# Kernel tuning notes

Measured on AMD Instinct MI355X. Metric: run time of the kernel, lower is better.

The kernel has to match this reference:

```python
import jax, jax.numpy as jnp
import numpy as np
from jax import lax

B, IN_C, Q_C, V_C, H, W = 16, 3, 8, 16, 224, 224
K = 7  # static conv kernel size


def _conv(x, w, stride=2, pad=3):
    # x: [N, Cin, H, W], w: [Cout, Cin, kh, kw]
    return lax.conv_general_dilated(
        x, w, (stride, stride), [(pad, pad), (pad, pad)],
        dimension_numbers=("NCHW", "OIHW", "NCHW"))


def _dyn_conv(inp, w):
    # per-sample dynamic conv: inp [C, H, W], w [O, C, kh, kw] -> [O, oh, ow]
    return _conv(inp[None], w, stride=2, pad=3)[0]


def setup_inputs() -> dict:
    key = jax.random.key(0)
    ks = jax.random.split(key, 8)
    x = jax.random.normal(ks[0], (B, IN_C, H, W), dtype=jnp.float32)
    # q_conv_params: input_channel x (weight [q, in, 7, 7], bias [q])
    Wq = jax.random.normal(ks[1], (IN_C, Q_C, IN_C, K, K), dtype=jnp.float32)
    bq = jax.random.normal(ks[2], (IN_C, Q_C), dtype=jnp.float32)
    # k_conv_paramss: input_channel x v_channel x (weight [q, in, 7, 7], bias [q])
    Wk = jax.random.normal(ks[3], (IN_C, V_C, Q_C, IN_C, K, K), dtype=jnp.float32)
    bk = jax.random.normal(ks[4], (IN_C, V_C, Q_C), dtype=jnp.float32)
    # v_conv_param: (weight [v, in, 7, 7], bias [v])
    Wv = jax.random.normal(ks[5], (V_C, IN_C, K, K), dtype=jnp.float32)
    bv = jax.random.normal(ks[6], (V_C,), dtype=jnp.float32)
    return {"x": x, "Wq": Wq, "bq": bq, "Wk": Wk, "bk": bk, "Wv": Wv, "bv": bv}


def reference(x, Wq, bq, Wk, bk, Wv, bv):
    b = x.shape[0]
    in_c, q_c = Wq.shape[0], Wq.shape[1]
    v_c = Wk.shape[1]
    # q: stack of input_channel static convs -> one grouped-by-output conv
    q = _conv(x, Wq.reshape(in_c * q_c, *Wq.shape[2:])) \
        + bq.reshape(-1)[None, :, None, None]
    h2, w2 = q.shape[-2], q.shape[-1]  # 112, 112
    q = q.reshape(b, in_c, q_c, h2, w2)
    # ks: input_channel x v_channel static convs fused into one conv
    kmap = _conv(x, Wk.reshape(in_c * v_c * q_c, *Wk.shape[3:])) \
        + bk.reshape(-1)[None, :, None, None]
    kmap = kmap.reshape(b, in_c, v_c, q_c, h2, w2)
    # a: per (batch, in_c) dynamic conv with feature maps as 112x112 kernels
    # input q[b,i] [q_c, h2, w2], weight kmap[b,i] [v_c, q_c, h2, w2] -> [v_c, 4, 4]
    a = jax.vmap(jax.vmap(_dyn_conv))(q, kmap)  # [B, in_c, v_c, 4, 4]
    # v: static conv
    v = _conv(x, Wv) + bv[None, :, None, None]  # [B, v_c, h2, w2]
    # o: per-batch dynamic conv with a[b] as kernel -> [B, in_c, 58, 58]
    o = jax.vmap(_dyn_conv)(v, a)
    return o
```

## Files before the change

### kernel.cpp

```cpp
#include <hip/hip_runtime.h>
#include <hip/hip_bf16.h>

#define BATCH 16
#define IN_C 3
#define Q_C 8
#define V_C 16
#define HH 224
#define WW 224
#define KK 7

#define XPH 230
#define XPW 232
#define QPH 118
#define QPW 120
#define QP_PLANE (QPH*QPW)
#define QP_QSTRIDE (Q_C*QP_PLANE)

#define PT_MB    202
#define PT2_CHUNKS (BATCH*IN_C*PT_MB*112)
#define PT2_N    ((size_t)PT2_CHUNKS*8)

#define PLANES_N (BATCH*7*IN_C*XPH*QPW)
#define VPAD_N   (BATCH*V_C*QPH*QPW)
#define QPADS_N  (BATCH*IN_C*QP_QSTRIDE)
#define D_N      (BATCH*160*384)
#define SPLITS   16
#define DPART_N  (SPLITS*D_N)
#define OUT_N    (BATCH*IN_C*58*58)
#define AW_N     (4*48*192)

#define ZQ_CHUNKS (BATCH*IN_C*Q_C*6*15)
#define ZV_CHUNKS (BATCH*V_C*6*30)

typedef __attribute__((ext_vector_type(8))) short bf16x8;
typedef __attribute__((ext_vector_type(4))) float f32x4;
typedef __attribute__((ext_vector_type(4))) unsigned short u16x4;

struct __attribute__((packed, aligned(4))) uint4_a4 { uint4 v; };
struct __attribute__((packed, aligned(4))) float4_a4 { float4 v; };

static __device__ inline unsigned short f2b(float f) {
    __hip_bfloat16 h = __float2bfloat16(f);
    return *reinterpret_cast<unsigned short*>(&h);
}
static __device__ inline float b2f(unsigned short u) {
    unsigned int v = ((unsigned int)u) << 16;
    return __builtin_bit_cast(float, v);
}
static __device__ inline bf16x8 ld16(const unsigned short* p) {
    return __builtin_bit_cast(bf16x8, *(const uint4*)p);
}

__global__ __launch_bounds__(256) void kXT(const float* __restrict__ x,
                                           unsigned short* __restrict__ planes,
                                           unsigned short* __restrict__ pT2) {
    int blk = blockIdx.x;
    int r0 = blk % 29;
    int t0 = blk / 29;
    int ci = t0 % IN_C;
    int b  = t0 / IN_C;
    int tid = threadIdx.x;

    __shared__ unsigned short xl[8][240];

    const float* xb = x + (size_t)(b * IN_C + ci) * (HH * WW);
    for (int idx = tid; idx < 8 * 240; idx += 256) {
        int row8 = idx / 240, c = idx % 240;
        int r = 8 * r0 + row8 - 3;
        int cc = c - 3;
        float val = 0.0f;
        if (r >= 0 && r < HH && cc >= 0 && cc < WW)
            val = xb[(size_t)r * WW + cc];
        xl[row8][c] = f2b(val);
    }
    __syncthreads();

    for (int t2 = tid; t2 < 840; t2 += 256) {
        int ko = t2 % 15;
        int t3 = t2 / 15;
        int row8 = t3 % 8;
        int dx = t3 / 8;
        int prow = 8 * r0 + row8;
        if (prow >= XPH) continue;
        unsigned short pk[8];
        if (ko < 14) {
            #pragma unroll
            for (int j = 0; j < 8; ++j)
                pk[j] = xl[row8][16 * ko + 2 * j + dx];
        } else {
            #pragma unroll
            for (int j = 0; j < 8; ++j) pk[j] = 0;
        }
        unsigned short* dst = planes
            + ((size_t)((b * 7 + dx) * IN_C + ci) * XPH + prow) * QPW + 8 * ko;
        *(uint4*)dst = *(const uint4*)pk;
    }

    for (int t2 = tid; t2 < 784; t2 += 256) {
        int kc  = t2 % 112;
        int mbr = t2 / 112;
        int mb = 7 * r0 + mbr;
        if (mb >= PT_MB) continue;
        unsigned short pk[8];
        #pragma unroll
        for (int j = 0; j < 8; ++j) {
            int mrel = 8 * mbr + j;
            int row8 = mrel / 7;
            int dxm  = mrel - 7 * row8;
            pk[j] = xl[row8][2 * kc + dxm];
        }
        unsigned short* dst = pT2 + ((size_t)((b * IN_C + ci) * PT_MB + mb) * 112 + kc) * 8;
        *(uint4*)dst = *(const uint4*)pk;
    }
}

__global__ __launch_bounds__(256) void kW(const float* __restrict__ Wq,
                                          const float* __restrict__ Wv,
                                          unsigned short* __restrict__ Aw2) {
    int idx = blockIdx.x * 256 + threadIdx.x;
    if (idx >= AW_N) return;
    int n = idx % 192;
    int t3 = idx / 192;
    int ch = t3 % 48;
    int p4 = t3 / 48;
    int ci = n / 64;
    int t  = (n % 64) - 2 * p4;
    float v = 0.0f;
    if (ch < 40 && t >= 0 && t < 49) {
        int k = ci * 49 + t;
        v = (ch < 24) ? Wq[(size_t)ch * 147 + k] : Wv[(size_t)(ch - 24) * 147 + k];
    }
    Aw2[idx] = f2b(v);
}

__global__ __launch_bounds__(256) void kZ(unsigned short* __restrict__ qpadS,
                                          float* __restrict__ vpad) {
    int idx = blockIdx.x * 256 + threadIdx.x;
    if (idx >= ZQ_CHUNKS + ZV_CHUNKS) return;
    uint4 z = uint4{0, 0, 0, 0};
    if (idx < ZQ_CHUNKS) {
        int ko = idx % 15;
        int t2 = idx / 15;
        int r6 = t2 % 6;
        int plane = t2 / 6;
        int row = (r6 < 3) ? r6 : (112 + r6);
        *(uint4*)(qpadS + (size_t)plane * QP_PLANE + (size_t)row * QPW + 8 * ko) = z;
    } else {
        int j = idx - ZQ_CHUNKS;
        int ko = j % 30;
        int t2 = j / 30;
        int r6 = t2 % 6;
        int plane = t2 / 6;
        int row = (r6 < 3) ? r6 : (112 + r6);
        *(uint4*)((char*)(vpad + (size_t)plane * QP_PLANE + (size_t)row * QPW) + 16 * ko) = z;
    }
}

__global__ __launch_bounds__(256) void kA(const unsigned short* __restrict__ pT2,
                                          const unsigned short* __restrict__ Aw2,
                                          const float* __restrict__ bq,
                                          const float* __restrict__ bv,
                                          unsigned short* __restrict__ qpadS,
                                          float* __restrict__ vpad) {
    int g = blockIdx.x;
    int r8 = g & 7, q8 = g >> 3;
    int b  = r8 + 8 * (q8 / 28);
    int yq = q8 % 28;
    int w  = threadIdx.x >> 6;
    int yo = yq * 4 + w;
    int lane = threadIdx.x & 63;
    int cl = lane & 15, kq = lane >> 4;

    __shared__ unsigned short qs[4][24][120];
    __shared__ float          vs[4][16][120];

    int m14 = 14 * yo;
    int p4  = (m14 >> 1) & 3;
    int ms8 = m14 >> 3;

    const unsigned short* AwP = Aw2 + (size_t)p4 * (48 * 192);
    bf16x8 af[3][6];
    #pragma unroll
    for (int mt = 0; mt < 3; ++mt)
        #pragma unroll
        for (int s = 0; s < 6; ++s)
            af[mt][s] = ld16(AwP + (size_t)(mt * 16 + cl) * 192 + s * 32 + kq * 8);

    f32x4 acc[3][7];
    #pragma unroll
    for (int mt = 0; mt < 3; ++mt)
        #pragma unroll
        for (int nt = 0; nt < 7; ++nt)
            acc[mt][nt] = f32x4{0.f, 0.f, 0.f, 0.f};

    #pragma unroll
    for (int s = 0; s < 6; ++s) {
        int ci = s >> 1;
        int mb = ms8 + kq + 4 * (s & 1);
        const unsigned short* bp = pT2
            + ((size_t)((b * IN_C + ci) * PT_MB + mb) * 112) * 8;
        bf16x8 bfr[7];
        #pragma unroll
        for (int nt = 0; nt < 7; ++nt)
            bfr[nt] = ld16(bp + (size_t)(nt * 16 + cl) * 8);
        #pragma unroll
        for (int nt = 0; nt < 7; ++nt)
            #pragma unroll
            for (int mt = 0; mt < 3; ++mt)
                acc[mt][nt] = __builtin_amdgcn_mfma_f32_16x16x32_bf16(af[mt][s], bfr[nt], acc[mt][nt], 0, 0, 0);
    }

    float bias[3][4];
    #pragma unroll
    for (int mt = 0; mt < 3; ++mt)
        #pragma unroll
        for (int r = 0; r < 4; ++r) {
            int ch = mt * 16 + kq * 4 + r;
            bias[mt][r] = (ch < 24) ? bq[ch] : (ch < 40 ? bv[ch - 24] : 0.0f);
        }

    for (int i = lane; i < 24 * 8; i += 64) {
        int ch = i / 8, c = i % 8;
        qs[w][ch][(c < 3) ? c : (112 + c)] = 0;
    }
    for (int i = lane; i < 16 * 8; i += 64) {
        int ch = i / 8, c = i % 8;
        vs[w][ch][(c < 3) ? c : (112 + c)] = 0.0f;
    }

    #pragma unroll
    for (int mt = 0; mt < 3; ++mt) {
        #pragma unroll
        for (int nt = 0; nt < 7; ++nt) {
            int kc = nt * 16 + cl;
            #pragma unroll
            for (int r = 0; r < 4; ++r) {
                int ch = mt * 16 + kq * 4 + r;
                float val = acc[mt][nt][r] + bias[mt][r];
                if (ch < 24) qs[w][ch][3 + kc] = f2b(val);
                else if (ch < 40) vs[w][ch - 24][3 + kc] = val;
            }
        }
    }
    __syncthreads();

    int orow = yo + 3;
    for (int i = lane; i < 24 * 15; i += 64) {
        int ch = i / 15, ko = i % 15;
        int icq = ch >> 3, qc = ch & 7;
        *(uint4*)(qpadS + (size_t)((b * 3 + icq) * 8 + qc) * QP_PLANE
                  + (size_t)orow * QPW + 8 * ko) = *(const uint4*)(&qs[w][ch][8 * ko]);
    }
    for (int i = lane; i < 16 * 30; i += 64) {
        int ch = i / 30, ko = i % 30;
        *(float4*)((char*)(vpad + (size_t)(b * 16 + ch) * QP_PLANE
                           + (size_t)orow * QPW) + 16 * ko) =
            *(const float4*)((const char*)(&vs[w][ch][0]) + 16 * ko);
    }
}

__global__ __launch_bounds__(512, 4) void kC(const unsigned short* __restrict__ planes,
                                             const unsigned short* __restrict__ qpadS,
                                             unsigned short* __restrict__ Dpart) {
    int blk = blockIdx.x;
    int b   = blk & 15;
    int nh  = (blk >> 4) & 1;
    int yc  = blk >> 5;
    int tid = threadIdx.x;
    int w = tid >> 6, lane = tid & 63;
    int tt = lane & 15, kq = lane >> 4;
    int th = tt >> 2, tw = tt & 3;

    __shared__ union {
        uint4 bs[80 * 17];
        unsigned short dq[80 * 392];
    } sm;

    int nreal = nh ? 67 : 80;

    if (tid < nreal * 3) {
        int nl = tid / 3, j2 = tid % 3;
        sm.bs[nl * 17 + 14 + j2] = uint4{0, 0, 0, 0};
    } else if (nh == 1) {
        int t2 = tid - nreal * 3;
        if (t2 < 13 * 17) {
            int nl = 67 + t2 / 17, ss = t2 % 17;
            uint4 v = (ss < 14) ? uint4{0x3F803F80u, 0x3F803F80u, 0x3F803F80u, 0x3F803F80u}
                                : uint4{0, 0, 0, 0};
            sm.bs[nl * 17 + ss] = v;
        }
    }

    int nch = nreal * 14;
    int soff[3];
    int sdst[3];
    bool sact[3];
    #pragma unroll
    for (int i = 0; i < 3; ++i) {
        int c = tid + 512 * i;
        sact[i] = (c < nch);
        int cc2 = sact[i] ? c : 0;
        int nl = cc2 / 14;
        int k0 = (cc2 % 14) * 8;
        int n = nh * 80 + nl;
        int ci = n / 49;
        int rr = n % 49;
        int dy = rr / 7;
        int dx = rr % 7;
        soff[i] = (((b * 7 + dx) * IN_C + ci) * XPH + dy) * QPW + k0;
        sdst[i] = nl * 17 + (k0 >> 3);
    }

    const unsigned short* abase[3];
    #pragma unroll
    for (int j = 0; j < 3; ++j) {
        int tile = w * 3 + j;
        int ic = tile >> 3, qc = tile & 7;
        abase[j] = qpadS + (size_t)(b * IN_C + ic) * QP_QSTRIDE + qc * QP_PLANE
                 + (2 * th) * QPW + 2 * tw;
    }

    f32x4 acc[3][5];
    #pragma unroll
    for (int j = 0; j < 3; ++j)
        #pragma unroll
        for (int nt = 0; nt < 5; ++nt)
            acc[j][nt] = f32x4{0.f, 0.f, 0.f, 0.f};

    uint4 pf[3];
    int yo0 = yc * 7;
    #pragma unroll
    for (int i = 0; i < 3; ++i)
        if (sact[i]) pf[i] = *(const uint4*)(planes + soff[i] + yo0 * 240);

    for (int ry = 0; ry < 7; ++ry) {
        int yo = yc * 7 + ry;
        __syncthreads();
        #pragma unroll
        for (int i = 0; i < 3; ++i)
            if (sact[i]) sm.bs[sdst[i]] = pf[i];
        __syncthreads();
        if (ry < 6) {
            #pragma unroll
            for (int i = 0; i < 3; ++i)
                if (sact[i]) pf[i] = *(const uint4*)(planes + soff[i] + (yo + 1) * 240);
        }
        #pragma unroll
        for (int s = 0; s < 4; ++s) {
            int k = 32 * s + kq * 8;
            int xs = (k < 112) ? k : 96;
            bf16x8 af[3];
            #pragma unroll
            for (int j = 0; j < 3; ++j)
                af[j] = __builtin_bit_cast(bf16x8,
                    ((const uint4_a4*)(abase[j] + yo * QPW + xs))->v);
            #pragma unroll
            for (int nt = 0; nt < 5; ++nt) {
                bf16x8 bf = __builtin_bit_cast(bf16x8, sm.bs[(nt * 16 + tt) * 17 + 4 * s + kq]);
                #pragma unroll
                for (int j = 0; j < 3; ++j)
                    acc[j][nt] = __builtin_amdgcn_mfma_f32_16x16x32_bf16(af[j], bf, acc[j][nt], 0, 0, 0);
            }
        }
    }

    __syncthreads();
    #pragma unroll
    for (int j = 0; j < 3; ++j) {
        int tile = w * 3 + j;
        int mb = tile * 16 + kq * 4;
        #pragma unroll
        for (int nt = 0; nt < 5; ++nt) {
            int nl = nt * 16 + tt;
            u16x4 pk;
            pk.x = f2b(acc[j][nt][0]);
            pk.y = f2b(acc[j][nt][1]);
            pk.z = f2b(acc[j][nt][2]);
            pk.w = f2b(acc[j][nt][3]);
            *(u16x4*)(&sm.dq[nl * 392 + mb]) = pk;
        }
    }
    __syncthreads();
    unsigned short* Dp = Dpart + (size_t)(yc * 16 + b) * (160 * 384);
    for (int c = tid; c < 80 * 48; c += 512) {
        int nl = c / 48, ms = c % 48;
        *(uint4*)(Dp + (size_t)(nh * 80 + nl) * 384 + ms * 8) =
            *(const uint4*)(&sm.dq[nl * 392 + ms * 8]);
    }
}

__global__ __launch_bounds__(256) void kR(const unsigned short* __restrict__ Dpart,
                                          float* __restrict__ Df) {
    int idx = blockIdx.x * 256 + threadIdx.x;
    float4 s = float4{0.f, 0.f, 0.f, 0.f};
    #pragma unroll
    for (int yc = 0; yc < SPLITS; ++yc) {
        u16x4 v = *(const u16x4*)(Dpart + (size_t)yc * D_N + 4 * (size_t)idx);
        s.x += b2f(v.x);
        s.y += b2f(v.y);
        s.z += b2f(v.z);
        s.w += b2f(v.w);
    }
    *(float4*)(Df + 4 * (size_t)idx) = s;
}

__global__ __launch_bounds__(256) void kE(const float* __restrict__ Df,
                                          const float* __restrict__ Wk,
                                          const float* __restrict__ bk,
                                          float* __restrict__ a_out) {
    int blk = blockIdx.x;
    int bi = blk >> 4;
    int v  = blk & 15;
    int ic = bi % IN_C;
    int b  = bi / IN_C;
    int tid = threadIdx.x;
    int t  = tid & 15;
    int rl = tid >> 4;
    const float* Dbase = Df + (size_t)b * (160 * 384);
    const float* WkI = Wk + (size_t)(ic * V_C + v) * (Q_C * 147);
    const float* bkI = bk + (ic * V_C + v) * Q_C;
    float s = 0.0f;
    for (int qc = 0; qc < Q_C; ++qc) {
        const float* wrow = WkI + qc * 147;
        int mcol = ic * 128 + qc * 16 + t;
        #pragma unroll
        for (int j = 0; j < 10; ++j) {
            int r = rl + 16 * j;
            if (r < 148) {
                float wv = (r < 147) ? wrow[r] : bkI[qc];
                s = fmaf(wv, Dbase[(size_t)r * 384 + mcol], s);
            }
        }
    }
    __shared__ float red[256];
    red[tid] = s;
    __syncthreads();
    if (tid < 16) {
        float acc2 = 0.f;
        #pragma unroll
        for (int k2 = 0; k2 < 16; ++k2) acc2 += red[k2 * 16 + tid];
        a_out[(size_t)blk * 16 + tid] = acc2;
    }
}

__global__ __launch_bounds__(256) void kO(const float* __restrict__ vpad,
                                          const float* __restrict__ a,
                                          float* __restrict__ out) {
    int idx = blockIdx.x * 256 + threadIdx.x;
    if (idx >= OUT_N) return;
    int ow = idx % 58;
    int t = idx / 58;
    int oh = t % 58; t /= 58;
    int ic = t % IN_C;
    int b  = t / IN_C;
    const float* ab = a + (size_t)(b * IN_C + ic) * (V_C * 16);
    float s = 0.0f;
    for (int vc = 0; vc < V_C; ++vc) {
        const float* vrow = vpad + ((size_t)(b * V_C + vc) * QPH + 2 * oh) * QPW + 2 * ow;
        const float* ar = ab + vc * 16;
        #pragma unroll
        for (int kh = 0; kh < 4; ++kh) {
            float4 xv = ((const float4_a4*)(vrow + kh * QPW))->v;
            s = fmaf(xv.x, ar[kh * 4 + 0], s);
            s = fmaf(xv.y, ar[kh * 4 + 1], s);
            s = fmaf(xv.z, ar[kh * 4 + 2], s);
            s = fmaf(xv.w, ar[kh * 4 + 3], s);
        }
    }
    out[idx] = s;
}

extern "C" void kernel_launch(void* const* d_in, const int* in_sizes, int n_in,
                              void* d_out, int out_size, void* d_ws, size_t ws_size,
                              hipStream_t stream) {
    (void)in_sizes; (void)n_in; (void)out_size; (void)ws_size;
    const float* x  = (const float*)d_in[0];
    const float* Wq = (const float*)d_in[1];
    const float* bq = (const float*)d_in[2];
    const float* Wk = (const float*)d_in[3];
    const float* bk = (const float*)d_in[4];
    const float* Wv = (const float*)d_in[5];
    const float* bv = (const float*)d_in[6];
    float* out = (float*)d_out;

    char* p = (char*)d_ws;
    unsigned short* pT2   = (unsigned short*)p;
    unsigned short* Dpart = (unsigned short*)p;
    p += (size_t)DPART_N * 2;
    unsigned short* planes = (unsigned short*)p;        p += (size_t)PLANES_N * 2;
    float*          vpad   = (float*)p;                 p += (size_t)VPAD_N * 4;
    unsigned short* qpadS  = (unsigned short*)p;        p += (size_t)QPADS_N * 2;
    float*          Df     = (float*)p;                 p += (size_t)D_N * 4;
    unsigned short* Aw2    = (unsigned short*)p;        p += (size_t)AW_N * 2;
    float*          a      = (float*)p;

    kXT<<<BATCH * IN_C * 29, 256, 0, stream>>>(x, planes, pT2);
    kW<<<(AW_N + 255) / 256, 256, 0, stream>>>(Wq, Wv, Aw2);
    kZ<<<(ZQ_CHUNKS + ZV_CHUNKS + 255) / 256, 256, 0, stream>>>(qpadS, vpad);
    kA<<<448, 256, 0, stream>>>(pT2, Aw2, bq, bv, qpadS, vpad);
    kC<<<SPLITS * 2 * 16, 512, 0, stream>>>(planes, qpadS, Dpart);
    kR<<<D_N / 4 / 256, 256, 0, stream>>>(Dpart, Df);
    kE<<<BATCH * IN_C * V_C, 256, 0, stream>>>(Df, Wk, bk, a);
    kO<<<(OUT_N + 255) / 256, 256, 0, stream>>>(vpad, a, out);
}
```

Baseline: 175.5 us.

## Double-buffer B rows in kC and merge weight-pack and zero-pad kernels

kC now stages two output rows of the plane data into shared memory per barrier pair, using a doubled LDS buffer. This cuts the number of __syncthreads in its 7-row loop from 14 to 8 and prefetches two rows at a time into registers. The kW and kZ setup kernels are also fused into one launch to remove a kernel launch. The costs are a larger shared-memory union (still bounded by the dq region), more prefetch registers in a 512-thread kernel that declares 4 blocks per SM, and slightly more complex control flow.

```diff
diff --git a/kernel.cpp b/kernel.cpp
--- a/kernel.cpp
+++ b/kernel.cpp
@@ -31,6 +31,7 @@
 
 #define ZQ_CHUNKS (BATCH*IN_C*Q_C*6*15)
 #define ZV_CHUNKS (BATCH*V_C*6*30)
+#define WZ_TOTAL  (AW_N + ZQ_CHUNKS + ZV_CHUNKS)
 
 typedef __attribute__((ext_vector_type(8))) short bf16x8;
 typedef __attribute__((ext_vector_type(4))) float f32x4;
@@ -114,41 +115,41 @@
     }
 }
 
-__global__ __launch_bounds__(256) void kW(const float* __restrict__ Wq,
-                                          const float* __restrict__ Wv,
-                                          unsigned short* __restrict__ Aw2) {
+__global__ __launch_bounds__(256) void kWZ(const float* __restrict__ Wq,
+                                           const float* __restrict__ Wv,
+                                           unsigned short* __restrict__ Aw2,
+                                           unsigned short* __restrict__ qpadS,
+                                           float* __restrict__ vpad) {
     int idx = blockIdx.x * 256 + threadIdx.x;
-    if (idx >= AW_N) return;
-    int n = idx % 192;
-    int t3 = idx / 192;
-    int ch = t3 % 48;
-    int p4 = t3 / 48;
-    int ci = n / 64;
-    int t  = (n % 64) - 2 * p4;
-    float v = 0.0f;
-    if (ch < 40 && t >= 0 && t < 49) {
-        int k = ci * 49 + t;
-        v = (ch < 24) ? Wq[(size_t)ch * 147 + k] : Wv[(size_t)(ch - 24) * 147 + k];
-    }
-    Aw2[idx] = f2b(v);
-}
-
-__global__ __launch_bounds__(256) void kZ(unsigned short* __restrict__ qpadS,
-                                          float* __restrict__ vpad) {
-    int idx = blockIdx.x * 256 + threadIdx.x;
-    if (idx >= ZQ_CHUNKS + ZV_CHUNKS) return;
+    if (idx >= WZ_TOTAL) return;
+    if (idx < AW_N) {
+        int n = idx % 192;
+        int t3 = idx / 192;
+        int ch = t3 % 48;
+        int p4 = t3 / 48;
+        int ci = n / 64;
+        int t  = (n % 64) - 2 * p4;
+        float v = 0.0f;
+        if (ch < 40 && t >= 0 && t < 49) {
+            int k = ci * 49 + t;
+            v = (ch < 24) ? Wq[(size_t)ch * 147 + k] : Wv[(size_t)(ch - 24) * 147 + k];
+        }
+        Aw2[idx] = f2b(v);
+        return;
+    }
     uint4 z = uint4{0, 0, 0, 0};
-    if (idx < ZQ_CHUNKS) {
-        int ko = idx % 15;
-        int t2 = idx / 15;
+    int j = idx - AW_N;
+    if (j < ZQ_CHUNKS) {
+        int ko = j % 15;
+        int t2 = j / 15;
         int r6 = t2 % 6;
         int plane = t2 / 6;
         int row = (r6 < 3) ? r6 : (112 + r6);
         *(uint4*)(qpadS + (size_t)plane * QP_PLANE + (size_t)row * QPW + 8 * ko) = z;
     } else {
-        int j = idx - ZQ_CHUNKS;
-        int ko = j % 30;
-        int t2 = j / 30;
+        int j2 = j - ZQ_CHUNKS;
+        int ko = j2 % 30;
+        int t2 = j2 / 30;
         int r6 = t2 % 6;
         int plane = t2 / 6;
         int row = (r6 < 3) ? r6 : (112 + r6);
@@ -272,7 +273,7 @@
     int th = tt >> 2, tw = tt & 3;
 
     __shared__ union {
-        uint4 bs[80 * 17];
+        uint4 bs[2 * 1360];
         unsigned short dq[80 * 392];
     } sm;
 
@@ -281,6 +282,7 @@
     if (tid < nreal * 3) {
         int nl = tid / 3, j2 = tid % 3;
         sm.bs[nl * 17 + 14 + j2] = uint4{0, 0, 0, 0};
+        sm.bs[1360 + nl * 17 + 14 + j2] = uint4{0, 0, 0, 0};
     } else if (nh == 1) {
         int t2 = tid - nreal * 3;
         if (t2 < 13 * 17) {
@@ -288,6 +290,7 @@
             uint4 v = (ss < 14) ? uint4{0x3F803F80u, 0x3F803F80u, 0x3F803F80u, 0x3F803F80u}
                                 : uint4{0, 0, 0, 0};
             sm.bs[nl * 17 + ss] = v;
+            sm.bs[1360 + nl * 17 + ss] = v;
         }
     }
 
@@ -327,39 +330,62 @@
         for (int nt = 0; nt < 5; ++nt)
             acc[j][nt] = f32x4{0.f, 0.f, 0.f, 0.f};
 
-    uint4 pf[3];
     int yo0 = yc * 7;
-    #pragma unroll
-    for (int i = 0; i < 3; ++i)
-        if (sact[i]) pf[i] = *(const uint4*)(planes + soff[i] + yo0 * 240);
-
-    for (int ry = 0; ry < 7; ++ry) {
-        int yo = yc * 7 + ry;
+    uint4 pf[6];
+    #pragma unroll
+    for (int i = 0; i < 3; ++i) {
+        if (sact[i]) {
+            pf[i]     = *(const uint4*)(planes + soff[i] + yo0 * 240);
+            pf[3 + i] = *(const uint4*)(planes + soff[i] + (yo0 + 1) * 240);
+        }
+    }
+
+    for (int rp = 0; rp < 4; ++rp) {
+        int yob = yo0 + 2 * rp;
+        int nload = (rp < 3) ? 2 : 1;
         __syncthreads();
         #pragma unroll
-        for (int i = 0; i < 3; ++i)
-            if (sact[i]) sm.bs[sdst[i]] = pf[i];
+        for (int rr = 0; rr < 2; ++rr) {
+            if (rr < nload) {
+                #pragma unroll
+                for (int i = 0; i < 3; ++i)
+                    if (sact[i]) sm.bs[rr * 1360 + sdst[i]] = pf[rr * 3 + i];
+            }
+        }
         __syncthreads();
-        if (ry < 6) {
+        if (rp < 3) {
+            int nnext = (rp < 2) ? 2 : 1;
             #pragma unroll
-            for (int i = 0; i < 3; ++i)
-                if (sact[i]) pf[i] = *(const uint4*)(planes + soff[i] + (yo + 1) * 240);
-        }
-        #pragma unroll
-        for (int s = 0; s < 4; ++s) {
-            int k = 32 * s + kq * 8;
-            int xs = (k < 112) ? k : 96;
-            bf16x8 af[3];
+            for (int rr = 0; rr < 2; ++rr) {
+                if (rr < nnext) {
+                    #pragma unroll
+                    for (int i = 0; i < 3; ++i)
+                        if (sact[i]) pf[rr * 3 + i] =
+                            *(const uint4*)(planes + soff[i] + (yob + 2 + rr) * 240);
+                }
+            }
+        }
+        #pragma unroll
+        for (int rr = 0; rr < 2; ++rr) {
+            if (rr >= nload) continue;
+            int yo = yob + rr;
+            const uint4* bsr = &sm.bs[rr * 1360];
             #pragma unroll
-            for (int j = 0; j < 3; ++j)
-                af[j] = __builtin_bit_cast(bf16x8,
-                    ((const uint4_a4*)(abase[j] + yo * QPW + xs))->v);
-            #pragma unroll
-            for (int nt = 0; nt < 5; ++nt) {
-                bf16x8 bf = __builtin_bit_cast(bf16x8, sm.bs[(nt * 16 + tt) * 17 + 4 * s + kq]);
+            for (int s = 0; s < 4; ++s) {
+                int k = 32 * s + kq * 8;
+                int xs = (k < 112) ? k : 96;
+                bf16x8 af[3];
                 #pragma unroll
                 for (int j = 0; j < 3; ++j)
-                    acc[j][nt] = __builtin_amdgcn_mfma_f32_16x16x32_bf16(af[j], bf, acc[j][nt], 0, 0, 0);
+                    af[j] = __builtin_bit_cast(bf16x8,
+                        ((const uint4_a4*)(abase[j] + yo * QPW + xs))->v);
+                #pragma unroll
+                for (int nt = 0; nt < 5; ++nt) {
+                    bf16x8 bf = __builtin_bit_cast(bf16x8, bsr[(nt * 16 + tt) * 17 + 4 * s + kq]);
+                    #pragma unroll
+                    for (int j = 0; j < 3; ++j)
+                        acc[j][nt] = __builtin_amdgcn_mfma_f32_16x16x32_bf16(af[j], bf, acc[j][nt], 0, 0, 0);
+                }
             }
         }
     }
@@ -495,8 +521,7 @@
     float*          a      = (float*)p;
 
     kXT<<<BATCH * IN_C * 29, 256, 0, stream>>>(x, planes, pT2);
-    kW<<<(AW_N + 255) / 256, 256, 0, stream>>>(Wq, Wv, Aw2);
-    kZ<<<(ZQ_CHUNKS + ZV_CHUNKS + 255) / 256, 256, 0, stream>>>(qpadS, vpad);
+    kWZ<<<(WZ_TOTAL + 255) / 256, 256, 0, stream>>>(Wq, Wv, Aw2, qpadS, vpad);
     kA<<<448, 256, 0, stream>>>(pT2, Aw2, bq, bv, qpadS, vpad);
     kC<<<SPLITS * 2 * 16, 512, 0, stream>>>(planes, qpadS, Dpart);
     kR<<<D_N / 4 / 256, 256, 0, stream>>>(Dpart, Df);
```

New measurement: 187.2 us. 6.7% more time.
